# Kernel optimization log

Measured on AMD Instinct MI355X. Metric: run time of the kernel, lower is better.

Reference implementation:

```python
import jax, jax.numpy as jnp
import numpy as np

N = 1024
H = 128


def setup_inputs() -> dict:
    key = jax.random.key(0)
    ks = jax.random.split(key, 12)
    s = 0.05
    inp = {
        "h": jax.random.normal(ks[0], (N, H), dtype=jnp.float32),
        "x": jax.random.normal(ks[1], (N, 2), dtype=jnp.float32),
        "batch": jnp.zeros((N,), dtype=jnp.int32),
        # attention projections (torch Linear: y = x @ W.T + b)
        "Wq": jax.random.normal(ks[2], (H, H), dtype=jnp.float32) * s,
        "bq": jnp.zeros((H,), dtype=jnp.float32),
        "Wk": jax.random.normal(ks[3], (H, H), dtype=jnp.float32) * s,
        "bk": jnp.zeros((H,), dtype=jnp.float32),
        "Wv": jax.random.normal(ks[4], (H, H), dtype=jnp.float32) * s,
        "bv": jnp.zeros((H,), dtype=jnp.float32),
        # edge_mlp: Linear(2,H) -> ReLU -> Linear(H,H)
        "We1": jax.random.normal(ks[5], (H, 2), dtype=jnp.float32) * s,
        "be1": jnp.zeros((H,), dtype=jnp.float32),
        "We2": jax.random.normal(ks[6], (H, H), dtype=jnp.float32) * s,
        "be2": jnp.zeros((H,), dtype=jnp.float32),
        # coord_mlp: Linear(H,1)
        "Wc": jax.random.normal(ks[7], (1, H), dtype=jnp.float32) * s,
        "bc": jnp.zeros((1,), dtype=jnp.float32),
    }
    return inp


def reference(h, x, batch, Wq, bq, Wk, bk, Wv, bv, We1, be1, We2, be2, Wc, bc):
    # rel_x[i, j] = x[i] - x[j]  -> [N, N, 2]
    rel_x = x[:, None, :] - x[None, :, :]
    # edge MLP over all pairs -> [N, N, H]
    edge_feat = jax.nn.relu(rel_x @ We1.T + be1) @ We2.T + be2
    q = h @ Wq.T + bq  # [N, H]
    k = h @ Wk.T + bk
    v = h @ Wv.T + bv
    scale = 1.0 / np.sqrt(float(H)).astype(np.float32)
    attn = jax.nn.softmax((q @ k.T) * scale, axis=-1)  # [N, N]
    agg_h = attn @ v  # [N, H]
    coord_w = edge_feat @ Wc.T + bc  # [N, N, 1]
    # weighted coordinate diffusion, summed over neighbors j (axis=1)
    delta_x = jnp.sum(attn[:, :, None] * (coord_w * rel_x), axis=1)  # [N, 2]
    return (h + agg_h, x + delta_x)
```

## Files before the change

### kernel.cpp

```cpp
#include <hip/hip_runtime.h>

#define NN 1024
#define HH 128
#define QR 2
#define RPB 4
#define TPB 512

__device__ __forceinline__ float4 wmax4(float4 v) {
#pragma unroll
  for (int off = 1; off < 64; off <<= 1) {
    v.x = fmaxf(v.x, __shfl_xor(v.x, off));
    v.y = fmaxf(v.y, __shfl_xor(v.y, off));
    v.z = fmaxf(v.z, __shfl_xor(v.z, off));
    v.w = fmaxf(v.w, __shfl_xor(v.w, off));
  }
  return v;
}

__device__ __forceinline__ float4 wsum4(float4 v) {
#pragma unroll
  for (int off = 1; off < 64; off <<= 1) {
    v.x += __shfl_xor(v.x, off);
    v.y += __shfl_xor(v.y, off);
    v.z += __shfl_xor(v.z, off);
    v.w += __shfl_xor(v.w, off);
  }
  return v;
}

__global__ __launch_bounds__(128)
void prep_kernel(const float* __restrict__ Wq, const float* __restrict__ Wk,
                 const float* __restrict__ Wv, const float* __restrict__ We1,
                 const float* __restrict__ be1, const float* __restrict__ We2,
                 const float* __restrict__ be2, const float* __restrict__ Wc,
                 const float* __restrict__ bc,
                 float* __restrict__ WqT, float* __restrict__ WkT,
                 float* __restrict__ WvT, float* __restrict__ epack,
                 float* __restrict__ c0) {
  const int d = blockIdx.x;
  const int o = threadIdx.x;
  WqT[d * HH + o] = Wq[o * HH + d];
  WkT[d * HH + o] = Wk[o * HH + d];
  WvT[d * HH + o] = Wv[o * HH + d];
  if (d == 0) {
    float uu = 0.f;
    for (int e = 0; e < HH; ++e) uu = fmaf(Wc[e], We2[e * HH + o], uu);
    epack[o * 4 + 0] = We1[2 * o];
    epack[o * 4 + 1] = We1[2 * o + 1];
    epack[o * 4 + 2] = be1[o];
    epack[o * 4 + 3] = uu;
    if (o == 0) {
      float s = bc[0];
      for (int e = 0; e < HH; ++e) s = fmaf(Wc[e], be2[e], s);
      c0[0] = s;
    }
  }
}

__global__ __launch_bounds__(128)
void qkv_kernel(const float* __restrict__ hin,
                const float* __restrict__ WqT, const float* __restrict__ WkT,
                const float* __restrict__ WvT,
                const float* __restrict__ bq, const float* __restrict__ bk,
                const float* __restrict__ bv,
                float* __restrict__ q, float* __restrict__ kT,
                float* __restrict__ v) {
  __shared__ __align__(16) float hT[HH][QR];
  const int tid = threadIdx.x;
  const int i0 = blockIdx.x * QR;
#pragma unroll
  for (int r = 0; r < QR; ++r) hT[tid][r] = hin[(i0 + r) * HH + tid];
  __syncthreads();
  float qa0 = 0.f, qa1 = 0.f, ka0 = 0.f, ka1 = 0.f, va0 = 0.f, va1 = 0.f;
#pragma unroll 4
  for (int d = 0; d < HH; ++d) {
    float wq = WqT[d * HH + tid];
    float wk = WkT[d * HH + tid];
    float wv = WvT[d * HH + tid];
    float2 hh = *(const float2*)&hT[d][0];
    qa0 = fmaf(hh.x, wq, qa0); qa1 = fmaf(hh.y, wq, qa1);
    ka0 = fmaf(hh.x, wk, ka0); ka1 = fmaf(hh.y, wk, ka1);
    va0 = fmaf(hh.x, wv, va0); va1 = fmaf(hh.y, wv, va1);
  }
  float bqv = bq[tid], bkv = bk[tid], bvv = bv[tid];
  q[(i0 + 0) * HH + tid] = qa0 + bqv;
  q[(i0 + 1) * HH + tid] = qa1 + bqv;
  v[(i0 + 0) * HH + tid] = va0 + bvv;
  v[(i0 + 1) * HH + tid] = va1 + bvv;
  float2 kk = make_float2(ka0 + bkv, ka1 + bkv);
  *(float2*)&kT[tid * NN + i0] = kk;
}

__global__ __launch_bounds__(TPB)
void fused_kernel(const float* __restrict__ q, const float* __restrict__ kT,
                  const float* __restrict__ v, const float* __restrict__ hin,
                  const float* __restrict__ x,
                  const float* __restrict__ epack, const float* __restrict__ c0p,
                  float* __restrict__ pws,
                  float* __restrict__ out_h, float* __restrict__ out_x) {
  __shared__ __align__(16) float sredh[8][RPB][HH];
  __shared__ __align__(16) float4 sredm[8];
  __shared__ __align__(16) float4 sreds[8];
  __shared__ __align__(16) float4 sredx[8];
  __shared__ __align__(16) float4 sredy[8];
  __shared__ __align__(16) float4 sinv;

  const int tid = threadIdx.x;
  const int lane = tid & 63;
  const int wid = tid >> 6;
  const int i0 = blockIdx.x * RPB;
  float* __restrict__ pblk = pws + (size_t)blockIdx.x * (NN * 4);

  float a00 = 0.f, a01 = 0.f, a02 = 0.f, a03 = 0.f;
  float a10 = 0.f, a11 = 0.f, a12 = 0.f, a13 = 0.f;
  const float2* kT2 = (const float2*)kT;
#pragma unroll 8
  for (int d = 0; d < HH; ++d) {
    float2 kk = kT2[d * (NN / 2) + tid];
    float q0 = q[(i0 + 0) * HH + d];
    float q1 = q[(i0 + 1) * HH + d];
    float q2 = q[(i0 + 2) * HH + d];
    float q3 = q[(i0 + 3) * HH + d];
    a00 = fmaf(q0, kk.x, a00); a10 = fmaf(q0, kk.y, a10);
    a01 = fmaf(q1, kk.x, a01); a11 = fmaf(q1, kk.y, a11);
    a02 = fmaf(q2, kk.x, a02); a12 = fmaf(q2, kk.y, a12);
    a03 = fmaf(q3, kk.x, a03); a13 = fmaf(q3, kk.y, a13);
  }
  const float scale = 0.08838834764831845f;
  float s00 = a00 * scale, s01 = a01 * scale, s02 = a02 * scale, s03 = a03 * scale;
  float s10 = a10 * scale, s11 = a11 * scale, s12 = a12 * scale, s13 = a13 * scale;

  float4 mv = make_float4(fmaxf(s00, s10), fmaxf(s01, s11),
                          fmaxf(s02, s12), fmaxf(s03, s13));
  mv = wmax4(mv);
  if (lane == 0) sredm[wid] = mv;
  __syncthreads();
  float4 mm = sredm[0];
#pragma unroll
  for (int w2 = 1; w2 < 8; ++w2) {
    float4 t4 = sredm[w2];
    mm.x = fmaxf(mm.x, t4.x); mm.y = fmaxf(mm.y, t4.y);
    mm.z = fmaxf(mm.z, t4.z); mm.w = fmaxf(mm.w, t4.w);
  }

  float e00 = __expf(s00 - mm.x), e01 = __expf(s01 - mm.y);
  float e02 = __expf(s02 - mm.z), e03 = __expf(s03 - mm.w);
  float e10 = __expf(s10 - mm.x), e11 = __expf(s11 - mm.y);
  float e12 = __expf(s12 - mm.z), e13 = __expf(s13 - mm.w);
  *(float4*)&pblk[(2 * tid) * 4]     = make_float4(e00, e01, e02, e03);
  *(float4*)&pblk[(2 * tid + 1) * 4] = make_float4(e10, e11, e12, e13);
  float4 sv = make_float4(e00 + e10, e01 + e11, e02 + e12, e03 + e13);
  sv = wsum4(sv);
  if (lane == 0) sreds[wid] = sv;
  __syncthreads();
  float4 ss = sreds[0];
#pragma unroll
  for (int w2 = 1; w2 < 8; ++w2) {
    float4 t4 = sreds[w2];
    ss.x += t4.x; ss.y += t4.y; ss.z += t4.z; ss.w += t4.w;
  }
  if (tid == 0)
    sinv = make_float4(1.f / ss.x, 1.f / ss.y, 1.f / ss.z, 1.f / ss.w);

  const int o2 = (tid & 63) * 2;
  const int sp = tid >> 6;
  float h00 = 0.f, h01 = 0.f, h02 = 0.f, h03 = 0.f;
  float h10 = 0.f, h11 = 0.f, h12 = 0.f, h13 = 0.f;
#pragma unroll 4
  for (int jj = 0; jj < NN / 8; ++jj) {
    int j = sp * (NN / 8) + jj;
    float2 vv = *(const float2*)&v[j * HH + o2];
    float4 pp = *(const float4*)&pblk[j * 4];
    h00 = fmaf(pp.x, vv.x, h00); h10 = fmaf(pp.x, vv.y, h10);
    h01 = fmaf(pp.y, vv.x, h01); h11 = fmaf(pp.y, vv.y, h11);
    h02 = fmaf(pp.z, vv.x, h02); h12 = fmaf(pp.z, vv.y, h12);
    h03 = fmaf(pp.w, vv.x, h03); h13 = fmaf(pp.w, vv.y, h13);
  }
  *(float2*)&sredh[sp][0][o2] = make_float2(h00, h10);
  *(float2*)&sredh[sp][1][o2] = make_float2(h01, h11);
  *(float2*)&sredh[sp][2][o2] = make_float2(h02, h12);
  *(float2*)&sredh[sp][3][o2] = make_float2(h03, h13);
  __syncthreads();
  {
    const int r = tid >> 7;
    const int o = tid & 127;
    float hv = 0.f;
#pragma unroll
    for (int s2 = 0; s2 < 8; ++s2) hv += sredh[s2][r][o];
    float invq = ((const float*)&sinv)[r];
    const int row = i0 + r;
    out_h[row * HH + o] = hin[row * HH + o] + hv * invq;
  }

  const int j0 = 2 * tid;
  float4 xx = *(const float4*)&x[j0 * 2];
  float xi0x = x[(i0 + 0) * 2 + 0], xi0y = x[(i0 + 0) * 2 + 1];
  float xi1x = x[(i0 + 1) * 2 + 0], xi1y = x[(i0 + 1) * 2 + 1];
  float xi2x = x[(i0 + 2) * 2 + 0], xi2y = x[(i0 + 2) * 2 + 1];
  float xi3x = x[(i0 + 3) * 2 + 0], xi3y = x[(i0 + 3) * 2 + 1];
  float dxa0 = xi0x - xx.x, dya0 = xi0y - xx.y;
  float dxa1 = xi1x - xx.x, dya1 = xi1y - xx.y;
  float dxa2 = xi2x - xx.x, dya2 = xi2y - xx.y;
  float dxa3 = xi3x - xx.x, dya3 = xi3y - xx.y;
  float dxb0 = xi0x - xx.z, dyb0 = xi0y - xx.w;
  float dxb1 = xi1x - xx.z, dyb1 = xi1y - xx.w;
  float dxb2 = xi2x - xx.z, dyb2 = xi2y - xx.w;
  float dxb3 = xi3x - xx.z, dyb3 = xi3y - xx.w;

  float wa0 = 0.f, wa1 = 0.f, wa2 = 0.f, wa3 = 0.f;
  float wb0 = 0.f, wb1 = 0.f, wb2 = 0.f, wb3 = 0.f;
  const float4* ep4 = (const float4*)epack;
#pragma unroll 4
  for (int t = 0; t < HH; ++t) {
    float4 e = ep4[t];
    float aa;
    aa = fmaxf(fmaf(e.x, dxa0, fmaf(e.y, dya0, e.z)), 0.f); wa0 = fmaf(e.w, aa, wa0);
    aa = fmaxf(fmaf(e.x, dxa1, fmaf(e.y, dya1, e.z)), 0.f); wa1 = fmaf(e.w, aa, wa1);
    aa = fmaxf(fmaf(e.x, dxa2, fmaf(e.y, dya2, e.z)), 0.f); wa2 = fmaf(e.w, aa, wa2);
    aa = fmaxf(fmaf(e.x, dxa3, fmaf(e.y, dya3, e.z)), 0.f); wa3 = fmaf(e.w, aa, wa3);
    aa = fmaxf(fmaf(e.x, dxb0, fmaf(e.y, dyb0, e.z)), 0.f); wb0 = fmaf(e.w, aa, wb0);
    aa = fmaxf(fmaf(e.x, dxb1, fmaf(e.y, dyb1, e.z)), 0.f); wb1 = fmaf(e.w, aa, wb1);
    aa = fmaxf(fmaf(e.x, dxb2, fmaf(e.y, dyb2, e.z)), 0.f); wb2 = fmaf(e.w, aa, wb2);
    aa = fmaxf(fmaf(e.x, dxb3, fmaf(e.y, dyb3, e.z)), 0.f); wb3 = fmaf(e.w, aa, wb3);
  }
  const float c0 = c0p[0];
  float cwa0 = e00 * (wa0 + c0), cwa1 = e01 * (wa1 + c0);
  float cwa2 = e02 * (wa2 + c0), cwa3 = e03 * (wa3 + c0);
  float cwb0 = e10 * (wb0 + c0), cwb1 = e11 * (wb1 + c0);
  float cwb2 = e12 * (wb2 + c0), cwb3 = e13 * (wb3 + c0);
  float4 rx = make_float4(fmaf(cwa0, dxa0, cwb0 * dxb0),
                          fmaf(cwa1, dxa1, cwb1 * dxb1),
                          fmaf(cwa2, dxa2, cwb2 * dxb2),
                          fmaf(cwa3, dxa3, cwb3 * dxb3));
  float4 ry = make_float4(fmaf(cwa0, dya0, cwb0 * dyb0),
                          fmaf(cwa1, dya1, cwb1 * dyb1),
                          fmaf(cwa2, dya2, cwb2 * dyb2),
                          fmaf(cwa3, dya3, cwb3 * dyb3));
  rx = wsum4(rx);
  ry = wsum4(ry);
  if (lane == 0) { sredx[wid] = rx; sredy[wid] = ry; }
  __syncthreads();
  if (tid < 4) {
    float sx = 0.f, sy = 0.f;
#pragma unroll
    for (int w2 = 0; w2 < 8; ++w2) {
      sx += ((const float*)sredx)[w2 * 4 + tid];
      sy += ((const float*)sredy)[w2 * 4 + tid];
    }
    float invr = ((const float*)&sinv)[tid];
    const int row = i0 + tid;
    out_x[row * 2 + 0] = x[row * 2 + 0] + sx * invr;
    out_x[row * 2 + 1] = x[row * 2 + 1] + sy * invr;
  }
}

extern "C" void kernel_launch(void* const* d_in, const int* in_sizes, int n_in,
                              void* d_out, int out_size, void* d_ws, size_t ws_size,
                              hipStream_t stream) {
  (void)in_sizes; (void)n_in; (void)out_size; (void)ws_size;
  const float* h   = (const float*)d_in[0];
  const float* x   = (const float*)d_in[1];
  const float* Wq  = (const float*)d_in[3];
  const float* bq  = (const float*)d_in[4];
  const float* Wk  = (const float*)d_in[5];
  const float* bk  = (const float*)d_in[6];
  const float* Wv  = (const float*)d_in[7];
  const float* bv  = (const float*)d_in[8];
  const float* We1 = (const float*)d_in[9];
  const float* be1 = (const float*)d_in[10];
  const float* We2 = (const float*)d_in[11];
  const float* be2 = (const float*)d_in[12];
  const float* Wc  = (const float*)d_in[13];
  const float* bc  = (const float*)d_in[14];

  float* ws  = (float*)d_ws;
  float* q_  = ws;
  float* kT  = q_ + NN * HH;
  float* v_  = kT + NN * HH;
  float* WqT = v_ + NN * HH;
  float* WkT = WqT + HH * HH;
  float* WvT = WkT + HH * HH;
  float* ep  = WvT + HH * HH;
  float* c0  = ep + 4 * HH;
  float* pws = c0 + 4;

  float* out_h = (float*)d_out;
  float* out_x = out_h + NN * HH;

  prep_kernel<<<dim3(HH), dim3(128), 0, stream>>>(
      Wq, Wk, Wv, We1, be1, We2, be2, Wc, bc, WqT, WkT, WvT, ep, c0);
  qkv_kernel<<<dim3(NN / QR), dim3(128), 0, stream>>>(
      h, WqT, WkT, WvT, bq, bk, bv, q_, kT, v_);
  fused_kernel<<<dim3(NN / RPB), dim3(TPB), 0, stream>>>(
      q_, kT, v_, h, x, ep, c0, pws, out_h, out_x);
}
```

Baseline: 143.1 us.

## Process one query row per block with probabilities kept in shared memory

Changes the fused attention kernel from four query rows per block to one row per block, launching 1024 blocks instead of 256. The softmax numerators are now stored in LDS rather than a global workspace, and the attention scale is folded into q inside the QKV kernel. This aims to raise occupancy across the GPU's compute units and drop the global scratch traffic. In exchange, each block must reload K and V for only one row, so K/V reuse per block falls by a factor of four and total cache traffic rises.

```diff
diff --git a/kernel.cpp b/kernel.cpp
--- a/kernel.cpp
+++ b/kernel.cpp
@@ -3,28 +3,16 @@
 #define NN 1024
 #define HH 128
 #define QR 2
-#define RPB 4
 #define TPB 512
 
-__device__ __forceinline__ float4 wmax4(float4 v) {
-#pragma unroll
-  for (int off = 1; off < 64; off <<= 1) {
-    v.x = fmaxf(v.x, __shfl_xor(v.x, off));
-    v.y = fmaxf(v.y, __shfl_xor(v.y, off));
-    v.z = fmaxf(v.z, __shfl_xor(v.z, off));
-    v.w = fmaxf(v.w, __shfl_xor(v.w, off));
-  }
+__device__ __forceinline__ float wmaxf(float v) {
+#pragma unroll
+  for (int off = 1; off < 64; off <<= 1) v = fmaxf(v, __shfl_xor(v, off));
   return v;
 }
-
-__device__ __forceinline__ float4 wsum4(float4 v) {
-#pragma unroll
-  for (int off = 1; off < 64; off <<= 1) {
-    v.x += __shfl_xor(v.x, off);
-    v.y += __shfl_xor(v.y, off);
-    v.z += __shfl_xor(v.z, off);
-    v.w += __shfl_xor(v.w, off);
-  }
+__device__ __forceinline__ float wsumf(float v) {
+#pragma unroll
+  for (int off = 1; off < 64; off <<= 1) v += __shfl_xor(v, off);
   return v;
 }
 
@@ -82,9 +70,10 @@
     ka0 = fmaf(hh.x, wk, ka0); ka1 = fmaf(hh.y, wk, ka1);
     va0 = fmaf(hh.x, wv, va0); va1 = fmaf(hh.y, wv, va1);
   }
+  const float scale = 0.08838834764831845f;
   float bqv = bq[tid], bkv = bk[tid], bvv = bv[tid];
-  q[(i0 + 0) * HH + tid] = qa0 + bqv;
-  q[(i0 + 1) * HH + tid] = qa1 + bqv;
+  q[(i0 + 0) * HH + tid] = (qa0 + bqv) * scale;
+  q[(i0 + 1) * HH + tid] = (qa1 + bqv) * scale;
   v[(i0 + 0) * HH + tid] = va0 + bvv;
   v[(i0 + 1) * HH + tid] = va1 + bvv;
   float2 kk = make_float2(ka0 + bkv, ka1 + bkv);
@@ -96,161 +85,96 @@
                   const float* __restrict__ v, const float* __restrict__ hin,
                   const float* __restrict__ x,
                   const float* __restrict__ epack, const float* __restrict__ c0p,
-                  float* __restrict__ pws,
                   float* __restrict__ out_h, float* __restrict__ out_x) {
-  __shared__ __align__(16) float sredh[8][RPB][HH];
-  __shared__ __align__(16) float4 sredm[8];
-  __shared__ __align__(16) float4 sreds[8];
-  __shared__ __align__(16) float4 sredx[8];
-  __shared__ __align__(16) float4 sredy[8];
-  __shared__ __align__(16) float4 sinv;
+  __shared__ __align__(16) float sp[NN];
+  __shared__ __align__(16) float sredh[8][HH];
+  __shared__ float sredm[8];
+  __shared__ float sreds[8];
+  __shared__ float sredx[8];
+  __shared__ float sredy[8];
 
   const int tid = threadIdx.x;
   const int lane = tid & 63;
   const int wid = tid >> 6;
-  const int i0 = blockIdx.x * RPB;
-  float* __restrict__ pblk = pws + (size_t)blockIdx.x * (NN * 4);
-
-  float a00 = 0.f, a01 = 0.f, a02 = 0.f, a03 = 0.f;
-  float a10 = 0.f, a11 = 0.f, a12 = 0.f, a13 = 0.f;
+  const int i = blockIdx.x;
+
+  float s0 = 0.f, s1 = 0.f;
   const float2* kT2 = (const float2*)kT;
 #pragma unroll 8
   for (int d = 0; d < HH; ++d) {
     float2 kk = kT2[d * (NN / 2) + tid];
-    float q0 = q[(i0 + 0) * HH + d];
-    float q1 = q[(i0 + 1) * HH + d];
-    float q2 = q[(i0 + 2) * HH + d];
-    float q3 = q[(i0 + 3) * HH + d];
-    a00 = fmaf(q0, kk.x, a00); a10 = fmaf(q0, kk.y, a10);
-    a01 = fmaf(q1, kk.x, a01); a11 = fmaf(q1, kk.y, a11);
-    a02 = fmaf(q2, kk.x, a02); a12 = fmaf(q2, kk.y, a12);
-    a03 = fmaf(q3, kk.x, a03); a13 = fmaf(q3, kk.y, a13);
-  }
-  const float scale = 0.08838834764831845f;
-  float s00 = a00 * scale, s01 = a01 * scale, s02 = a02 * scale, s03 = a03 * scale;
-  float s10 = a10 * scale, s11 = a11 * scale, s12 = a12 * scale, s13 = a13 * scale;
-
-  float4 mv = make_float4(fmaxf(s00, s10), fmaxf(s01, s11),
-                          fmaxf(s02, s12), fmaxf(s03, s13));
-  mv = wmax4(mv);
+    float qd = q[i * HH + d];
+    s0 = fmaf(qd, kk.x, s0);
+    s1 = fmaf(qd, kk.y, s1);
+  }
+
+  float mv = wmaxf(fmaxf(s0, s1));
   if (lane == 0) sredm[wid] = mv;
   __syncthreads();
-  float4 mm = sredm[0];
-#pragma unroll
-  for (int w2 = 1; w2 < 8; ++w2) {
-    float4 t4 = sredm[w2];
-    mm.x = fmaxf(mm.x, t4.x); mm.y = fmaxf(mm.y, t4.y);
-    mm.z = fmaxf(mm.z, t4.z); mm.w = fmaxf(mm.w, t4.w);
-  }
-
-  float e00 = __expf(s00 - mm.x), e01 = __expf(s01 - mm.y);
-  float e02 = __expf(s02 - mm.z), e03 = __expf(s03 - mm.w);
-  float e10 = __expf(s10 - mm.x), e11 = __expf(s11 - mm.y);
-  float e12 = __expf(s12 - mm.z), e13 = __expf(s13 - mm.w);
-  *(float4*)&pblk[(2 * tid) * 4]     = make_float4(e00, e01, e02, e03);
-  *(float4*)&pblk[(2 * tid + 1) * 4] = make_float4(e10, e11, e12, e13);
-  float4 sv = make_float4(e00 + e10, e01 + e11, e02 + e12, e03 + e13);
-  sv = wsum4(sv);
+  float mm = sredm[0];
+#pragma unroll
+  for (int w2 = 1; w2 < 8; ++w2) mm = fmaxf(mm, sredm[w2]);
+
+  float e0 = __expf(s0 - mm), e1 = __expf(s1 - mm);
+  *(float2*)&sp[2 * tid] = make_float2(e0, e1);
+  float sv = wsumf(e0 + e1);
   if (lane == 0) sreds[wid] = sv;
   __syncthreads();
-  float4 ss = sreds[0];
-#pragma unroll
-  for (int w2 = 1; w2 < 8; ++w2) {
-    float4 t4 = sreds[w2];
-    ss.x += t4.x; ss.y += t4.y; ss.z += t4.z; ss.w += t4.w;
-  }
-  if (tid == 0)
-    sinv = make_float4(1.f / ss.x, 1.f / ss.y, 1.f / ss.z, 1.f / ss.w);
+  float ss = sreds[0];
+#pragma unroll
+  for (int w2 = 1; w2 < 8; ++w2) ss += sreds[w2];
+  const float inv = 1.f / ss;
 
   const int o2 = (tid & 63) * 2;
-  const int sp = tid >> 6;
-  float h00 = 0.f, h01 = 0.f, h02 = 0.f, h03 = 0.f;
-  float h10 = 0.f, h11 = 0.f, h12 = 0.f, h13 = 0.f;
+  const int spn = tid >> 6;
+  float h0 = 0.f, h1 = 0.f;
 #pragma unroll 4
   for (int jj = 0; jj < NN / 8; ++jj) {
-    int j = sp * (NN / 8) + jj;
+    int j = spn * (NN / 8) + jj;
     float2 vv = *(const float2*)&v[j * HH + o2];
-    float4 pp = *(const float4*)&pblk[j * 4];
-    h00 = fmaf(pp.x, vv.x, h00); h10 = fmaf(pp.x, vv.y, h10);
-    h01 = fmaf(pp.y, vv.x, h01); h11 = fmaf(pp.y, vv.y, h11);
-    h02 = fmaf(pp.z, vv.x, h02); h12 = fmaf(pp.z, vv.y, h12);
-    h03 = fmaf(pp.w, vv.x, h03); h13 = fmaf(pp.w, vv.y, h13);
-  }
-  *(float2*)&sredh[sp][0][o2] = make_float2(h00, h10);
-  *(float2*)&sredh[sp][1][o2] = make_float2(h01, h11);
-  *(float2*)&sredh[sp][2][o2] = make_float2(h02, h12);
-  *(float2*)&sredh[sp][3][o2] = make_float2(h03, h13);
-  __syncthreads();
-  {
-    const int r = tid >> 7;
-    const int o = tid & 127;
-    float hv = 0.f;
-#pragma unroll
-    for (int s2 = 0; s2 < 8; ++s2) hv += sredh[s2][r][o];
-    float invq = ((const float*)&sinv)[r];
-    const int row = i0 + r;
-    out_h[row * HH + o] = hin[row * HH + o] + hv * invq;
-  }
-
-  const int j0 = 2 * tid;
-  float4 xx = *(const float4*)&x[j0 * 2];
-  float xi0x = x[(i0 + 0) * 2 + 0], xi0y = x[(i0 + 0) * 2 + 1];
-  float xi1x = x[(i0 + 1) * 2 + 0], xi1y = x[(i0 + 1) * 2 + 1];
-  float xi2x = x[(i0 + 2) * 2 + 0], xi2y = x[(i0 + 2) * 2 + 1];
-  float xi3x = x[(i0 + 3) * 2 + 0], xi3y = x[(i0 + 3) * 2 + 1];
-  float dxa0 = xi0x - xx.x, dya0 = xi0y - xx.y;
-  float dxa1 = xi1x - xx.x, dya1 = xi1y - xx.y;
-  float dxa2 = xi2x - xx.x, dya2 = xi2y - xx.y;
-  float dxa3 = xi3x - xx.x, dya3 = xi3y - xx.y;
-  float dxb0 = xi0x - xx.z, dyb0 = xi0y - xx.w;
-  float dxb1 = xi1x - xx.z, dyb1 = xi1y - xx.w;
-  float dxb2 = xi2x - xx.z, dyb2 = xi2y - xx.w;
-  float dxb3 = xi3x - xx.z, dyb3 = xi3y - xx.w;
-
-  float wa0 = 0.f, wa1 = 0.f, wa2 = 0.f, wa3 = 0.f;
-  float wb0 = 0.f, wb1 = 0.f, wb2 = 0.f, wb3 = 0.f;
+    float pp = sp[j];
+    h0 = fmaf(pp, vv.x, h0);
+    h1 = fmaf(pp, vv.y, h1);
+  }
+  *(float2*)&sredh[spn][o2] = make_float2(h0, h1);
+
+  float4 xx = *(const float4*)&x[4 * tid];
+  float xix = x[i * 2 + 0], xiy = x[i * 2 + 1];
+  float dxa = xix - xx.x, dya = xiy - xx.y;
+  float dxb = xix - xx.z, dyb = xiy - xx.w;
+  float wa = 0.f, wb = 0.f;
   const float4* ep4 = (const float4*)epack;
 #pragma unroll 4
   for (int t = 0; t < HH; ++t) {
     float4 e = ep4[t];
-    float aa;
-    aa = fmaxf(fmaf(e.x, dxa0, fmaf(e.y, dya0, e.z)), 0.f); wa0 = fmaf(e.w, aa, wa0);
-    aa = fmaxf(fmaf(e.x, dxa1, fmaf(e.y, dya1, e.z)), 0.f); wa1 = fmaf(e.w, aa, wa1);
-    aa = fmaxf(fmaf(e.x, dxa2, fmaf(e.y, dya2, e.z)), 0.f); wa2 = fmaf(e.w, aa, wa2);
-    aa = fmaxf(fmaf(e.x, dxa3, fmaf(e.y, dya3, e.z)), 0.f); wa3 = fmaf(e.w, aa, wa3);
-    aa = fmaxf(fmaf(e.x, dxb0, fmaf(e.y, dyb0, e.z)), 0.f); wb0 = fmaf(e.w, aa, wb0);
-    aa = fmaxf(fmaf(e.x, dxb1, fmaf(e.y, dyb1, e.z)), 0.f); wb1 = fmaf(e.w, aa, wb1);
-    aa = fmaxf(fmaf(e.x, dxb2, fmaf(e.y, dyb2, e.z)), 0.f); wb2 = fmaf(e.w, aa, wb2);
-    aa = fmaxf(fmaf(e.x, dxb3, fmaf(e.y, dyb3, e.z)), 0.f); wb3 = fmaf(e.w, aa, wb3);
+    float aa = fmaxf(fmaf(e.x, dxa, fmaf(e.y, dya, e.z)), 0.f);
+    wa = fmaf(e.w, aa, wa);
+    float bb = fmaxf(fmaf(e.x, dxb, fmaf(e.y, dyb, e.z)), 0.f);
+    wb = fmaf(e.w, bb, wb);
   }
   const float c0 = c0p[0];
-  float cwa0 = e00 * (wa0 + c0), cwa1 = e01 * (wa1 + c0);
-  float cwa2 = e02 * (wa2 + c0), cwa3 = e03 * (wa3 + c0);
-  float cwb0 = e10 * (wb0 + c0), cwb1 = e11 * (wb1 + c0);
-  float cwb2 = e12 * (wb2 + c0), cwb3 = e13 * (wb3 + c0);
-  float4 rx = make_float4(fmaf(cwa0, dxa0, cwb0 * dxb0),
-                          fmaf(cwa1, dxa1, cwb1 * dxb1),
-                          fmaf(cwa2, dxa2, cwb2 * dxb2),
-                          fmaf(cwa3, dxa3, cwb3 * dxb3));
-  float4 ry = make_float4(fmaf(cwa0, dya0, cwb0 * dyb0),
-                          fmaf(cwa1, dya1, cwb1 * dyb1),
-                          fmaf(cwa2, dya2, cwb2 * dyb2),
-                          fmaf(cwa3, dya3, cwb3 * dyb3));
-  rx = wsum4(rx);
-  ry = wsum4(ry);
+  float cwa = e0 * (wa + c0);
+  float cwb = e1 * (wb + c0);
+  float rx = fmaf(cwa, dxa, cwb * dxb);
+  float ry = fmaf(cwa, dya, cwb * dyb);
+  rx = wsumf(rx);
+  ry = wsumf(ry);
   if (lane == 0) { sredx[wid] = rx; sredy[wid] = ry; }
-  __syncthreads();
-  if (tid < 4) {
+
+  __syncthreads();
+
+  if (tid < HH) {
+    float hv = 0.f;
+#pragma unroll
+    for (int s2 = 0; s2 < 8; ++s2) hv += sredh[s2][tid];
+    out_h[i * HH + tid] = hin[i * HH + tid] + hv * inv;
+  }
+  if (tid == 0) {
     float sx = 0.f, sy = 0.f;
 #pragma unroll
-    for (int w2 = 0; w2 < 8; ++w2) {
-      sx += ((const float*)sredx)[w2 * 4 + tid];
-      sy += ((const float*)sredy)[w2 * 4 + tid];
-    }
-    float invr = ((const float*)&sinv)[tid];
-    const int row = i0 + tid;
-    out_x[row * 2 + 0] = x[row * 2 + 0] + sx * invr;
-    out_x[row * 2 + 1] = x[row * 2 + 1] + sy * invr;
+    for (int w2 = 0; w2 < 8; ++w2) { sx += sredx[w2]; sy += sredy[w2]; }
+    out_x[i * 2 + 0] = x[i * 2 + 0] + sx * inv;
+    out_x[i * 2 + 1] = x[i * 2 + 1] + sy * inv;
   }
 }
 
@@ -282,7 +206,6 @@
   float* WvT = WkT + HH * HH;
   float* ep  = WvT + HH * HH;
   float* c0  = ep + 4 * HH;
-  float* pws = c0 + 4;
 
   float* out_h = (float*)d_out;
   float* out_x = out_h + NN * HH;
@@ -291,6 +214,6 @@
       Wq, Wk, Wv, We1, be1, We2, be2, Wc, bc, WqT, WkT, WvT, ep, c0);
   qkv_kernel<<<dim3(NN / QR), dim3(128), 0, stream>>>(
       h, WqT, WkT, WvT, bq, bk, bv, q_, kT, v_);
-  fused_kernel<<<dim3(NN / RPB), dim3(TPB), 0, stream>>>(
-      q_, kT, v_, h, x, ep, c0, pws, out_h, out_x);
-}
+  fused_kernel<<<dim3(NN), dim3(TPB), 0, stream>>>(
+      q_, kT, v_, h, x, ep, c0, out_h, out_x);
+}
```

Measured after the change: 164.1 us. +14.7%, slower.
